# Performance work log

Hardware: AMD Instinct MI355X
Metric: run time of the kernel (lower is better)

## Reference

```python
import jax, jax.numpy as jnp
import numpy as np

K = 10
EPS = 1e-5

def leaky(x):
    return jnp.where(x >= 0, x, 0.2 * x)

def graph_feature(x, k):
    # x: (B, C, N) -> edge features (B, 2C, N, k), standard DGCNN get_graph_feature
    B, C, N = x.shape
    xx = jnp.sum(x * x, axis=1)                      # (B, N)
    inner = jnp.einsum('bcn,bcm->bnm', x, x)          # (B, N, N)
    pair = 2.0 * inner - xx[:, :, None] - xx[:, None, :]  # -||xi - xj||^2
    _, idx = jax.lax.top_k(pair, k)                   # (B, N, k)
    xt = jnp.transpose(x, (0, 2, 1))                  # (B, N, C)
    nbr = xt[jnp.arange(B)[:, None, None], idx]       # (B, N, k, C) gather
    ctr = jnp.broadcast_to(xt[:, :, None, :], nbr.shape)
    feat = jnp.concatenate([nbr - ctr, ctr], axis=-1)  # (B, N, k, 2C)
    return jnp.transpose(feat, (0, 3, 1, 2))          # (B, 2C, N, k)

def edge_block(x, W, k):
    # gather -> 1x1 conv (edge MLP) -> leaky relu -> max over neighbors
    e = graph_feature(x, k)                           # (B, 2C, N, k)
    h = leaky(jnp.einsum('oc,bcnk->bonk', W, e))      # (B, O, N, k)
    return jnp.max(h, axis=-1)                        # (B, O, N)

def bn(x, g, b, m, v):
    # inference batchnorm over channel axis 1; x: (B, C, ...) 
    shape = (1, -1) + (1,) * (x.ndim - 2)
    return (x - m.reshape(shape)) * (g.reshape(shape) * jax.lax.rsqrt(v.reshape(shape) + EPS)) + b.reshape(shape)

def setup_inputs() -> dict:
    key = jax.random.key(0)
    ks = jax.random.split(key, 20)
    s = lambda i, shape, scale: (jax.random.normal(ks[i], shape, jnp.float32) * scale)
    inp = {
        'input': jax.random.normal(ks[0], (759, 220, 3), jnp.float32),
        'W1': s(1, (32, 6), 0.4),
        'W2': s(2, (32, 64), 0.15),
        'W3': s(3, (64, 64), 0.15),
        'W4': s(4, (128, 128), 0.1),
        'W5': s(5, (512, 256), 0.08),
        'g5': 1.0 + s(6, (512,), 0.05), 'b5': s(7, (512,), 0.05),
        'm5': s(8, (512,), 0.05), 'v5': 1.0 + 0.1 * jax.random.uniform(ks[9], (512,), jnp.float32),
        'Wl1': s(10, (1024, 1024), 0.03),
        'g6': 1.0 + s(11, (1024,), 0.05), 'b6': s(12, (1024,), 0.05),
        'm6': s(13, (1024,), 0.05), 'v6': 1.0 + 0.1 * jax.random.uniform(ks[14], (1024,), jnp.float32),
        'Wl2': s(15, (380, 1024), 0.03),
        'bl2': s(16, (380,), 0.02),
    }
    return inp

def reference(input, W1, W2, W3, W4, W5, g5, b5, m5, v5, Wl1, g6, b6, m6, v6, Wl2, bl2):
    x = jnp.transpose(input.reshape(-1, 220, 3), (0, 2, 1))  # (B, 3, N)
    x1 = edge_block(x, W1, K)    # (B, 32, N)
    x2 = edge_block(x1, W2, K)   # (B, 32, N)
    x3 = edge_block(x2, W3, K)   # (B, 64, N)
    x4 = edge_block(x3, W4, K)   # (B, 128, N)
    xc = jnp.concatenate([x1, x2, x3, x4], axis=1)           # (B, 256, N)
    h = leaky(bn(jnp.einsum('oc,bcn->bon', W5, xc), g5, b5, m5, v5))  # (B, 512, N)
    p = jnp.concatenate([jnp.max(h, axis=-1), jnp.mean(h, axis=-1)], axis=1)  # (B, 1024)
    z = leaky(bn(p @ Wl1.T, g6, b6, m6, v6))  # dropout is identity in eval
    return z @ Wl2.T + bl2                     # (B, 380)
```

## Files before the change

### kernel.cpp

```cpp
#include <hip/hip_runtime.h>
#include <math.h>

#define NB 759
#define NPT 220
#define KNN 10
#define XCCH 256
#define LDXC (XCCH * NPT)

typedef float f4 __attribute__((ext_vector_type(4)));
typedef float f16v __attribute__((ext_vector_type(16)));
typedef short bf8v __attribute__((ext_vector_type(8)));

__device__ inline unsigned short bfh(float x) {
  unsigned u = __float_as_uint(x);
  unsigned r = u + 0x7FFFu + ((u >> 16) & 1u);
  return (unsigned short)(r >> 16);
}
__device__ inline float bff(unsigned short h) {
  return __uint_as_float(((unsigned)h) << 16);
}
__device__ inline void bfsplit(float x, unsigned short& h, unsigned short& l) {
  h = bfh(x);
  l = bfh(x - bff(h));
}

__global__ __launch_bounds__(256) void k_transpose(const float* __restrict__ in, float* __restrict__ x0) {
  int i = blockIdx.x * 256 + threadIdx.x;
  if (i >= NB * 3 * NPT) return;
  int n = i % NPT; int t = i / NPT; int c = t % 3; int b = t / 3;
  x0[i] = in[(b * NPT + n) * 3 + c];
}

__global__ __launch_bounds__(256) void k_w5split(const float* __restrict__ W5,
    unsigned short* __restrict__ Wh, unsigned short* __restrict__ Wl) {
  int i = blockIdx.x * 256 + threadIdx.x;
  if (i >= 512 * 256) return;
  bfsplit(W5[i], Wh[i], Wl[i]);
}

__device__ inline void topk_insert(float d, int m, float* tv, int* ti) {
  if (d > tv[KNN - 1]) {
    tv[KNN - 1] = d; ti[KNN - 1] = m;
    #pragma unroll
    for (int j = KNN - 1; j >= 1; --j) {
      if (tv[j] > tv[j - 1]) {
        float tf = tv[j - 1]; tv[j - 1] = tv[j]; tv[j] = tf;
        int tq = ti[j - 1]; ti[j - 1] = ti[j]; ti[j] = tq;
      } else break;
    }
  }
}

__global__ __launch_bounds__(256) void k_knn3(const float* __restrict__ x, int ldb,
                                              int* __restrict__ idxout) {
  __shared__ __align__(16) float xl[NPT * 4];
  __shared__ float xx[NPT];
  int b = blockIdx.x;
  const float* xb = x + (size_t)b * ldb;
  for (int i = threadIdx.x; i < NPT; i += 256) {
    f4 v; v.x = xb[i]; v.y = xb[NPT + i]; v.z = xb[2 * NPT + i]; v.w = 0.f;
    *(f4*)&xl[i * 4] = v;
    xx[i] = v.x * v.x + v.y * v.y + v.z * v.z;
  }
  __syncthreads();
  int n = threadIdx.x;
  if (n >= NPT) return;
  f4 xn = *(const f4*)&xl[n * 4];
  float xxn = xx[n];
  float tv[KNN]; int ti[KNN];
  #pragma unroll
  for (int k = 0; k < KNN; ++k) { tv[k] = -1e30f; ti[k] = 0; }
  for (int m = 0; m < NPT; ++m) {
    f4 v = *(const f4*)&xl[m * 4];
    float dot = xn.x * v.x + xn.y * v.y + xn.z * v.z;
    topk_insert(2.f * dot - xxn - xx[m], m, tv, ti);
  }
  int* ib = idxout + ((size_t)b * NPT + n) * KNN;
  #pragma unroll
  for (int k = 0; k < KNN; ++k) ib[k] = ti[k];
}

template<int C>
__global__ __launch_bounds__(512) void k_knn_mfma(const float* __restrict__ x, int ldb,
                                                  int* __restrict__ idxout) {
  constexpr int KPG = C + 8;
  constexpr int SW = (C / 16) - 1;
  __shared__ __align__(16) unsigned short XH[224 * KPG];
  __shared__ __align__(16) unsigned short XM[224 * KPG];
  __shared__ __align__(16) unsigned short XL[224 * KPG];
  __shared__ float xx[224];
  int b = blockIdx.x;
  const float* xb = x + (size_t)b * ldb;
  for (int i = threadIdx.x; i < C * 224; i += 512) {
    int c = i / 224, m = i - c * 224;
    float v = (m < NPT) ? xb[c * NPT + m] : 0.f;
    unsigned short h = bfh(v);
    float r1 = v - bff(h);
    unsigned short mm = bfh(r1);
    unsigned short l = bfh(r1 - bff(mm));
    int cs = c ^ ((m & SW) << 4);
    XH[m * KPG + cs] = h; XM[m * KPG + cs] = mm; XL[m * KPG + cs] = l;
  }
  for (int m = threadIdx.x; m < 224; m += 512) {
    float s = 0.f;
    if (m < NPT) {
      for (int c = 0; c < C; ++c) { float v = xb[c * NPT + m]; s += v * v; }
    } else s = 1e30f;
    xx[m] = s;
  }
  __syncthreads();
  int w = threadIdx.x >> 6;
  int lane = threadIdx.x & 63;
  int lc = lane & 31, hi = lane >> 5;
  float tv[KNN]; int ti[KNN];
  #pragma unroll
  for (int k = 0; k < KNN; ++k) { tv[k] = -1e30f; ti[k] = 0; }
  if (w < 7) {
    int n = w * 32 + lc;
    f16v acc[7];
    #pragma unroll
    for (int mt = 0; mt < 7; ++mt)
      #pragma unroll
      for (int i = 0; i < 16; ++i) acc[mt][i] = 0.f;
    #pragma unroll
    for (int ks = 0; ks < C / 16; ++ks) {
      int kb = ks * 16 + hi * 8;
      int nsw = kb ^ ((n & SW) << 4);
      bf8v bh = *(const bf8v*)&XH[n * KPG + nsw];
      bf8v bm = *(const bf8v*)&XM[n * KPG + nsw];
      bf8v bl = *(const bf8v*)&XL[n * KPG + nsw];
      #pragma unroll
      for (int mt = 0; mt < 7; ++mt) {
        int mr = mt * 32 + lc;
        int msw = kb ^ ((mr & SW) << 4);
        bf8v ah = *(const bf8v*)&XH[mr * KPG + msw];
        bf8v am = *(const bf8v*)&XM[mr * KPG + msw];
        bf8v al = *(const bf8v*)&XL[mr * KPG + msw];
        acc[mt] = __builtin_amdgcn_mfma_f32_32x32x16_bf16(ah, bh, acc[mt], 0, 0, 0);
        acc[mt] = __builtin_amdgcn_mfma_f32_32x32x16_bf16(am, bh, acc[mt], 0, 0, 0);
        acc[mt] = __builtin_amdgcn_mfma_f32_32x32x16_bf16(ah, bm, acc[mt], 0, 0, 0);
        acc[mt] = __builtin_amdgcn_mfma_f32_32x32x16_bf16(am, bm, acc[mt], 0, 0, 0);
        acc[mt] = __builtin_amdgcn_mfma_f32_32x32x16_bf16(al, bh, acc[mt], 0, 0, 0);
        acc[mt] = __builtin_amdgcn_mfma_f32_32x32x16_bf16(ah, bl, acc[mt], 0, 0, 0);
      }
    }
    float xxn = xx[n];
    #pragma unroll
    for (int mt = 0; mt < 7; ++mt)
      #pragma unroll
      for (int i = 0; i < 16; ++i) {
        int m = mt * 32 + (i & 3) + 8 * (i >> 2) + 4 * hi;
        float d = 2.f * acc[mt][i] - xx[m] - xxn;
        topk_insert(d, m, tv, ti);
      }
  }
  __syncthreads();
  float* LV = (float*)XH;
  int* LI = (int*)XM;
  if (w < 7) {
    int slot = (w * 64 + lane) * KNN;
    #pragma unroll
    for (int k = 0; k < KNN; ++k) { LV[slot + k] = tv[k]; LI[slot + k] = ti[k]; }
  }
  __syncthreads();
  if (w < 7 && hi == 0) {
    int n = w * 32 + lc;
    if (n < NPT) {
      int sa = (w * 64 + lane) * KNN, sb = sa + 32 * KNN;
      int a = 0, bq = 0;
      int* ob = idxout + ((size_t)b * NPT + n) * KNN;
      #pragma unroll
      for (int k = 0; k < KNN; ++k) {
        float va = LV[sa + a], vb = LV[sb + bq];
        int ia = LI[sa + a], ic = LI[sb + bq];
        bool ta = (va > vb) || (va == vb && ia < ic);
        ob[k] = ta ? ia : ic;
        if (ta) ++a; else ++bq;
      }
    }
  }
}

template<int CIN>
__global__ __launch_bounds__(256, 2) void k_conv_fused(const float* __restrict__ x, int ldb,
    const float* __restrict__ W, const int* __restrict__ idxb, float* __restrict__ xout) {
  constexpr int NPAD = 224;
  constexpr int DBS = 224;
  constexpr int REGION = 64 * DBS;
  __shared__ __align__(16) float smem[REGION + CIN * 64];
  __shared__ unsigned short idxl[NPT * KNN];
  float* xl = smem;
  float* db = smem;
  float* wl = smem + REGION;
  int b = blockIdx.x, og = blockIdx.y;
  const float* xb = x + (size_t)b * ldb;
  for (int i = threadIdx.x; i < CIN * NPAD; i += 256) {
    int c = i / NPAD, n = i - c * NPAD;
    xl[i] = (n < NPT) ? xb[c * NPT + n] : 0.f;
  }
  for (int i = threadIdx.x; i < 64 * CIN; i += 256) {
    int rl = i & 63, c = i >> 6;
    int o = og * 32 + (rl & 31);
    float wv = (rl < 32) ? W[o * 2 * CIN + c]
                         : (W[o * 2 * CIN + CIN + c] - W[o * 2 * CIN + c]);
    wl[c * 64 + rl] = wv;
  }
  for (int i = threadIdx.x; i < NPT * KNN; i += 256)
    idxl[i] = (unsigned short)idxb[(size_t)b * NPT * KNN + i];
  __syncthreads();
  int rq = threadIdx.x & 15, nq = threadIdx.x >> 4;
  int gv[4]; bool gok[4];
  #pragma unroll
  for (int j = 0; j < 4; ++j) { int g = nq + j * 16; gok[j] = g < 55; gv[j] = (g < 55 ? g : 54) * 4; }
  f4 acc[4][4];
  #pragma unroll
  for (int j = 0; j < 4; ++j)
    #pragma unroll
    for (int i2 = 0; i2 < 4; ++i2) acc[j][i2] = (f4){0.f, 0.f, 0.f, 0.f};
  #pragma unroll 2
  for (int c = 0; c < CIN; ++c) {
    f4 wv = *(const f4*)&wl[c * 64 + rq * 4];
    #pragma unroll
    for (int j = 0; j < 4; ++j) {
      f4 xv = *(const f4*)&xl[c * NPAD + gv[j]];
      acc[j][0] += wv.x * xv; acc[j][1] += wv.y * xv;
      acc[j][2] += wv.z * xv; acc[j][3] += wv.w * xv;
    }
  }
  __syncthreads();
  #pragma unroll
  for (int j = 0; j < 4; ++j) {
    if (gok[j]) {
      #pragma unroll
      for (int i2 = 0; i2 < 4; ++i2)
        *(f4*)&db[(rq * 4 + i2) * DBS + gv[j]] = acc[j][i2];
    }
  }
  __syncthreads();
  int o0 = og * 32;
  for (int i = threadIdx.x; i < 32 * NPT; i += 256) {
    int ol = i / NPT, n = i - ol * NPT;
    const float* drow = &db[ol * DBS];
    const unsigned short* ib = &idxl[n * KNN];
    float mx = -1e30f;
    #pragma unroll
    for (int k = 0; k < KNN; ++k) mx = fmaxf(mx, drow[ib[k]]);
    float v = mx + db[(32 + ol) * DBS + n];
    xout[((size_t)b * XCCH + o0 + ol) * NPT + n] = (v >= 0.f) ? v : 0.2f * v;
  }
}

#define KP 72
__global__ __launch_bounds__(256) void k_w5_mfma(const float* __restrict__ xc,
    const unsigned short* __restrict__ Wh, const unsigned short* __restrict__ Wl,
    const float* __restrict__ g5, const float* __restrict__ b5, const float* __restrict__ m5,
    const float* __restrict__ v5, float* __restrict__ p) {
  __shared__ __align__(16) unsigned short XH[224 * KP];
  __shared__ __align__(16) unsigned short XL[224 * KP];
  int d = blockIdx.x;
  int b = (d & 7) * 95 + (d >> 5);
  int rg = (d >> 3) & 3;
  if (b >= NB) return;
  int lane = threadIdx.x & 63, w = threadIdx.x >> 6;
  f16v acc[7];
  #pragma unroll
  for (int t = 0; t < 7; ++t)
    #pragma unroll
    for (int i = 0; i < 16; ++i) acc[t][i] = 0.f;

  int r = rg * 128 + w * 32 + (lane & 31);
  int khalf = (lane >> 5) * 8;

  for (int cb = 0; cb < 4; ++cb) {
    if (cb) __syncthreads();
    for (int i = threadIdx.x; i < 32 * NPT; i += 256) {
      int cp = i / NPT;
      int n = i - cp * NPT;
      int c0 = cp * 2;
      const float* src = &xc[((size_t)b * XCCH + cb * 64 + c0) * NPT + n];
      float x0 = src[0];
      float x1 = src[NPT];
      unsigned short h0, l0, h1, l1;
      bfsplit(x0, h0, l0); bfsplit(x1, h1, l1);
      ((unsigned*)XH)[(n * KP + c0) >> 1] = (unsigned)h0 | ((unsigned)h1 << 16);
      ((unsigned*)XL)[(n * KP + c0) >> 1] = (unsigned)l0 | ((unsigned)l1 << 16);
    }
    for (int i = threadIdx.x; i < 4 * 32; i += 256) {
      int n = NPT + (i >> 5); int cd = i & 31;
      ((unsigned*)XH)[n * (KP / 2) + cd] = 0u;
      ((unsigned*)XL)[n * (KP / 2) + cd] = 0u;
    }
    __syncthreads();
    #pragma unroll
    for (int ks = 0; ks < 4; ++ks) {
      int kg = cb * 64 + ks * 16 + khalf;
      int kl = ks * 16 + khalf;
      bf8v ah = *(const bf8v*)&Wh[(size_t)r * 256 + kg];
      bf8v al = *(const bf8v*)&Wl[(size_t)r * 256 + kg];
      #pragma unroll
      for (int t = 0; t < 7; ++t) {
        int col = t * 32 + (lane & 31);
        bf8v bh = *(const bf8v*)&XH[col * KP + kl];
        bf8v bl = *(const bf8v*)&XL[col * KP + kl];
        acc[t] = __builtin_amdgcn_mfma_f32_32x32x16_bf16(ah, bh, acc[t], 0, 0, 0);
        acc[t] = __builtin_amdgcn_mfma_f32_32x32x16_bf16(al, bh, acc[t], 0, 0, 0);
        acc[t] = __builtin_amdgcn_mfma_f32_32x32x16_bf16(ah, bl, acc[t], 0, 0, 0);
      }
    }
  }
  int rbase = rg * 128 + w * 32 + 4 * (lane >> 5);
  int lc = lane & 31;
  #pragma unroll
  for (int i = 0; i < 16; ++i) {
    int row = rbase + (i & 3) + 8 * (i >> 2);
    float a = g5[row] * rsqrtf(v5[row] + 1e-5f);
    float dq = b5[row] - m5[row] * a;
    float mx = -1e30f, sm = 0.f;
    #pragma unroll
    for (int t = 0; t < 7; ++t) {
      bool valid = (t < 6) || (lc < 28);
      float hv = a * acc[t][i] + dq;
      float lv = (hv >= 0.f) ? hv : 0.2f * hv;
      if (valid) { mx = fmaxf(mx, lv); sm += lv; }
    }
    #pragma unroll
    for (int m_ = 1; m_ <= 16; m_ <<= 1) {
      mx = fmaxf(mx, __shfl_xor(mx, m_));
      sm += __shfl_xor(sm, m_);
    }
    if (lc == 0) {
      p[(size_t)b * 1024 + row] = mx;
      p[(size_t)b * 1024 + 512 + row] = sm * (1.f / NPT);
    }
  }
}

template<int ON, bool FUSE>
__global__ __launch_bounds__(256) void k_fc(const float* __restrict__ in, const float* __restrict__ Wt,
    const float* __restrict__ q0, const float* __restrict__ q1, const float* __restrict__ q2,
    const float* __restrict__ q3, float* __restrict__ out, int ostride) {
  __shared__ __align__(16) float il[32 * 68];
  __shared__ __align__(16) float wl[32 * 68];
  int b0 = blockIdx.x * 64, o0 = blockIdx.y * 64;
  int oq = threadIdx.x & 15, bq = threadIdx.x >> 4;
  f4 acc[4];
  #pragma unroll
  for (int i2 = 0; i2 < 4; ++i2) acc[i2] = (f4){0.f, 0.f, 0.f, 0.f};
  for (int cb = 0; cb < 32; ++cb) {
    if (cb) __syncthreads();
    for (int i = threadIdx.x; i < 2048; i += 256) {
      int c = i & 31, bb = i >> 5;
      il[c * 68 + bb] = (b0 + bb < NB) ? in[(b0 + bb) * 1024 + cb * 32 + c] : 0.f;
    }
    for (int i = threadIdx.x; i < 2048; i += 256) {
      int c = i & 31, ol = i >> 5;
      wl[c * 68 + ol] = (o0 + ol < ON) ? Wt[(o0 + ol) * 1024 + cb * 32 + c] : 0.f;
    }
    __syncthreads();
    #pragma unroll
    for (int c = 0; c < 32; ++c) {
      f4 wv = *(const f4*)&wl[c * 68 + oq * 4];
      f4 iv = *(const f4*)&il[c * 68 + bq * 4];
      acc[0] += wv.x * iv; acc[1] += wv.y * iv; acc[2] += wv.z * iv; acc[3] += wv.w * iv;
    }
  }
  #pragma unroll
  for (int i2 = 0; i2 < 4; ++i2) {
    int o = o0 + oq * 4 + i2;
    if (o >= ON) continue;
    float A = 1.f, Dv = 0.f;
    if (FUSE) { float a = q0[o] * rsqrtf(q3[o] + 1e-5f); A = a; Dv = q1[o] - q2[o] * a; }
    else { Dv = q0[o]; }
    #pragma unroll
    for (int jj = 0; jj < 4; ++jj) {
      int bb = b0 + bq * 4 + jj;
      if (bb < NB) {
        float v = acc[i2][jj];
        if (FUSE) { v = A * v + Dv; v = (v >= 0.f) ? v : 0.2f * v; }
        else { v = v + Dv; }
        out[(size_t)bb * ostride + o] = v;
      }
    }
  }
}

extern "C" void kernel_launch(void* const* d_in, const int* in_sizes, int n_in,
                              void* d_out, int out_size, void* d_ws, size_t ws_size,
                              hipStream_t stream) {
  const float* input = (const float*)d_in[0];
  const float* W1 = (const float*)d_in[1];
  const float* W2 = (const float*)d_in[2];
  const float* W3 = (const float*)d_in[3];
  const float* W4 = (const float*)d_in[4];
  const float* W5 = (const float*)d_in[5];
  const float* g5 = (const float*)d_in[6];
  const float* b5 = (const float*)d_in[7];
  const float* m5 = (const float*)d_in[8];
  const float* v5 = (const float*)d_in[9];
  const float* Wl1 = (const float*)d_in[10];
  const float* g6 = (const float*)d_in[11];
  const float* b6 = (const float*)d_in[12];
  const float* m6 = (const float*)d_in[13];
  const float* v6 = (const float*)d_in[14];
  const float* Wl2 = (const float*)d_in[15];
  const float* bl2 = (const float*)d_in[16];

  float* w = (float*)d_ws;
  float* x0 = w;
  float* xc = x0 + 500940;
  float* p  = xc + 42746880;
  float* z  = p  + 777216;
  int* idxb = (int*)(z + 777216);
  unsigned short* wh = (unsigned short*)(w + 46472052);
  unsigned short* wlo = wh + 131072;

  k_transpose<<<1957, 256, 0, stream>>>(input, x0);
  k_w5split<<<512, 256, 0, stream>>>(W5, wh, wlo);

  k_knn3<<<759, 256, 0, stream>>>(x0, 3 * NPT, idxb);
  k_conv_fused<3><<<dim3(759, 1), 256, 0, stream>>>(x0, 3 * NPT, W1, idxb, xc);

  k_knn_mfma<32><<<759, 512, 0, stream>>>(xc, LDXC, idxb);
  k_conv_fused<32><<<dim3(759, 1), 256, 0, stream>>>(xc, LDXC, W2, idxb, xc + 32 * NPT);

  k_knn_mfma<32><<<759, 512, 0, stream>>>(xc + 32 * NPT, LDXC, idxb);
  k_conv_fused<32><<<dim3(759, 2), 256, 0, stream>>>(xc + 32 * NPT, LDXC, W3, idxb, xc + 64 * NPT);

  k_knn_mfma<64><<<759, 512, 0, stream>>>(xc + 64 * NPT, LDXC, idxb);
  k_conv_fused<64><<<dim3(759, 4), 256, 0, stream>>>(xc + 64 * NPT, LDXC, W4, idxb, xc + 128 * NPT);

  k_w5_mfma<<<3040, 256, 0, stream>>>(xc, wh, wlo, g5, b5, m5, v5, p);

  k_fc<1024, true><<<dim3(12, 16), 256, 0, stream>>>(p, Wl1, g6, b6, m6, v6, z, 1024);
  k_fc<380, false><<<dim3(12, 6), 256, 0, stream>>>(z, Wl2, bl2, bl2, bl2, bl2, (float*)d_out, 380);
}
```

Baseline: 1.698 ms.

## Restructure W5 MFMA kernel: 512 threads, waves split over columns, swizzled LDS

The W5 pointwise-conv kernel now runs 512 threads per block. Each of 7 active waves owns one 32-column slice of points and loops over 4 row tiles, where before each of 4 waves owned a row slice and swept all 7 column tiles. The padded LDS layout (KP=72) becomes an XOR-swizzled 64-wide layout to avoid bank conflicts. BN scale and shift are precomputed once into shared memory, and the max/mean reduction is finished through a shared buffer across waves. This cuts accumulator registers per wave and reuses each LDS B fragment across 4 row tiles. In exchange, one of the 8 waves sits idle during compute, W fragments are reloaded from global memory more often, and an extra sync plus shared-memory reduction is added.

```diff
diff --git a/kernel.cpp b/kernel.cpp
--- a/kernel.cpp
+++ b/kernel.cpp
@@ -250,30 +250,37 @@
   }
 }
 
-#define KP 72
-__global__ __launch_bounds__(256) void k_w5_mfma(const float* __restrict__ xc,
+__global__ __launch_bounds__(512, 4) void k_w5_mfma(const float* __restrict__ xc,
     const unsigned short* __restrict__ Wh, const unsigned short* __restrict__ Wl,
     const float* __restrict__ g5, const float* __restrict__ b5, const float* __restrict__ m5,
     const float* __restrict__ v5, float* __restrict__ p) {
-  __shared__ __align__(16) unsigned short XH[224 * KP];
-  __shared__ __align__(16) unsigned short XL[224 * KP];
+  __shared__ __align__(16) unsigned short XH[224 * 64];
+  __shared__ __align__(16) unsigned short XL[224 * 64];
+  __shared__ float red[128][8][2];
+  __shared__ float ADq[128][2];
   int d = blockIdx.x;
   int b = (d & 7) * 95 + (d >> 5);
   int rg = (d >> 3) & 3;
   if (b >= NB) return;
   int lane = threadIdx.x & 63, w = threadIdx.x >> 6;
-  f16v acc[7];
-  #pragma unroll
-  for (int t = 0; t < 7; ++t)
-    #pragma unroll
-    for (int i = 0; i < 16; ++i) acc[t][i] = 0.f;
-
-  int r = rg * 128 + w * 32 + (lane & 31);
-  int khalf = (lane >> 5) * 8;
+  int lc = lane & 31, hi = lane >> 5;
+
+  if (threadIdx.x < 128) {
+    int row = rg * 128 + threadIdx.x;
+    float a = g5[row] * rsqrtf(v5[row] + 1e-5f);
+    ADq[threadIdx.x][0] = a;
+    ADq[threadIdx.x][1] = b5[row] - m5[row] * a;
+  }
+
+  f16v acc[4];
+  #pragma unroll
+  for (int rt = 0; rt < 4; ++rt)
+    #pragma unroll
+    for (int i = 0; i < 16; ++i) acc[rt][i] = 0.f;
 
   for (int cb = 0; cb < 4; ++cb) {
     if (cb) __syncthreads();
-    for (int i = threadIdx.x; i < 32 * NPT; i += 256) {
+    for (int i = threadIdx.x; i < 32 * NPT; i += 512) {
       int cp = i / NPT;
       int n = i - cp * NPT;
       int c0 = cp * 2;
@@ -282,56 +289,71 @@
       float x1 = src[NPT];
       unsigned short h0, l0, h1, l1;
       bfsplit(x0, h0, l0); bfsplit(x1, h1, l1);
-      ((unsigned*)XH)[(n * KP + c0) >> 1] = (unsigned)h0 | ((unsigned)h1 << 16);
-      ((unsigned*)XL)[(n * KP + c0) >> 1] = (unsigned)l0 | ((unsigned)l1 << 16);
-    }
-    for (int i = threadIdx.x; i < 4 * 32; i += 256) {
+      int dw = n * 32 + (((c0 >> 3) ^ (n & 7)) << 2) + ((c0 & 7) >> 1);
+      ((unsigned*)XH)[dw] = (unsigned)h0 | ((unsigned)h1 << 16);
+      ((unsigned*)XL)[dw] = (unsigned)l0 | ((unsigned)l1 << 16);
+    }
+    for (int i = threadIdx.x; i < 128; i += 512) {
       int n = NPT + (i >> 5); int cd = i & 31;
-      ((unsigned*)XH)[n * (KP / 2) + cd] = 0u;
-      ((unsigned*)XL)[n * (KP / 2) + cd] = 0u;
+      ((unsigned*)XH)[n * 32 + cd] = 0u;
+      ((unsigned*)XL)[n * 32 + cd] = 0u;
     }
     __syncthreads();
-    #pragma unroll
-    for (int ks = 0; ks < 4; ++ks) {
-      int kg = cb * 64 + ks * 16 + khalf;
-      int kl = ks * 16 + khalf;
-      bf8v ah = *(const bf8v*)&Wh[(size_t)r * 256 + kg];
-      bf8v al = *(const bf8v*)&Wl[(size_t)r * 256 + kg];
-      #pragma unroll
-      for (int t = 0; t < 7; ++t) {
-        int col = t * 32 + (lane & 31);
-        bf8v bh = *(const bf8v*)&XH[col * KP + kl];
-        bf8v bl = *(const bf8v*)&XL[col * KP + kl];
-        acc[t] = __builtin_amdgcn_mfma_f32_32x32x16_bf16(ah, bh, acc[t], 0, 0, 0);
-        acc[t] = __builtin_amdgcn_mfma_f32_32x32x16_bf16(al, bh, acc[t], 0, 0, 0);
-        acc[t] = __builtin_amdgcn_mfma_f32_32x32x16_bf16(ah, bl, acc[t], 0, 0, 0);
-      }
-    }
-  }
-  int rbase = rg * 128 + w * 32 + 4 * (lane >> 5);
-  int lc = lane & 31;
-  #pragma unroll
-  for (int i = 0; i < 16; ++i) {
-    int row = rbase + (i & 3) + 8 * (i >> 2);
-    float a = g5[row] * rsqrtf(v5[row] + 1e-5f);
-    float dq = b5[row] - m5[row] * a;
+    if (w < 7) {
+      int col = w * 32 + lc;
+      int swc = col & 7;
+      const unsigned short* XHr = &XH[col * 64];
+      const unsigned short* XLr = &XL[col * 64];
+      #pragma unroll
+      for (int ks = 0; ks < 4; ++ks) {
+        int gr = (((ks * 2 + hi) ^ swc) << 3);
+        bf8v bh = *(const bf8v*)&XHr[gr];
+        bf8v bl = *(const bf8v*)&XLr[gr];
+        int kg = cb * 64 + ks * 16 + hi * 8;
+        const unsigned short* wp = Wh + (size_t)(rg * 128 + lc) * 256 + kg;
+        const unsigned short* wq = Wl + (size_t)(rg * 128 + lc) * 256 + kg;
+        #pragma unroll
+        for (int rt = 0; rt < 4; ++rt) {
+          bf8v ah = *(const bf8v*)(wp + rt * 32 * 256);
+          bf8v al = *(const bf8v*)(wq + rt * 32 * 256);
+          acc[rt] = __builtin_amdgcn_mfma_f32_32x32x16_bf16(ah, bh, acc[rt], 0, 0, 0);
+          acc[rt] = __builtin_amdgcn_mfma_f32_32x32x16_bf16(al, bh, acc[rt], 0, 0, 0);
+          acc[rt] = __builtin_amdgcn_mfma_f32_32x32x16_bf16(ah, bl, acc[rt], 0, 0, 0);
+        }
+      }
+    }
+  }
+  if (w < 7) {
+    bool allv = (w < 6);
+    #pragma unroll
+    for (int rt = 0; rt < 4; ++rt) {
+      #pragma unroll
+      for (int i = 0; i < 16; ++i) {
+        int rl = rt * 32 + (i & 3) + 8 * (i >> 2) + 4 * hi;
+        float a = ADq[rl][0], dq = ADq[rl][1];
+        float hv = a * acc[rt][i] + dq;
+        float lv = (hv >= 0.f) ? hv : 0.2f * hv;
+        bool valid = allv || (lc < 28);
+        float mx = valid ? lv : -1e30f;
+        float sm = valid ? lv : 0.f;
+        #pragma unroll
+        for (int m_ = 1; m_ <= 16; m_ <<= 1) {
+          mx = fmaxf(mx, __shfl_xor(mx, m_));
+          sm += __shfl_xor(sm, m_);
+        }
+        if (lc == 0) { red[rl][w][0] = mx; red[rl][w][1] = sm; }
+      }
+    }
+  }
+  __syncthreads();
+  if (threadIdx.x < 128) {
+    int rl = threadIdx.x;
     float mx = -1e30f, sm = 0.f;
     #pragma unroll
-    for (int t = 0; t < 7; ++t) {
-      bool valid = (t < 6) || (lc < 28);
-      float hv = a * acc[t][i] + dq;
-      float lv = (hv >= 0.f) ? hv : 0.2f * hv;
-      if (valid) { mx = fmaxf(mx, lv); sm += lv; }
-    }
-    #pragma unroll
-    for (int m_ = 1; m_ <= 16; m_ <<= 1) {
-      mx = fmaxf(mx, __shfl_xor(mx, m_));
-      sm += __shfl_xor(sm, m_);
-    }
-    if (lc == 0) {
-      p[(size_t)b * 1024 + row] = mx;
-      p[(size_t)b * 1024 + 512 + row] = sm * (1.f / NPT);
-    }
+    for (int q = 0; q < 7; ++q) { mx = fmaxf(mx, red[rl][q][0]); sm += red[rl][q][1]; }
+    int row = rg * 128 + rl;
+    p[(size_t)b * 1024 + row] = mx;
+    p[(size_t)b * 1024 + 512 + row] = sm * (1.f / NPT);
   }
 }
 
@@ -429,7 +451,7 @@
   k_knn_mfma<64><<<759, 512, 0, stream>>>(xc + 64 * NPT, LDXC, idxb);
   k_conv_fused<64><<<dim3(759, 4), 256, 0, stream>>>(xc + 64 * NPT, LDXC, W4, idxb, xc + 128 * NPT);
 
-  k_w5_mfma<<<3040, 256, 0, stream>>>(xc, wh, wlo, g5, b5, m5, v5, p);
+  k_w5_mfma<<<3040, 512, 0, stream>>>(xc, wh, wlo, g5, b5, m5, v5, p);
 
   k_fc<1024, true><<<dim3(12, 16), 256, 0, stream>>>(p, Wl1, g6, b6, m6, v6, z, 1024);
   k_fc<380, false><<<dim3(12, 6), 256, 0, stream>>>(z, Wl2, bl2, bl2, bl2, bl2, (float*)d_out, 380);
```

Result: slower. 1.901 ms (+11.9%).

## Emit pre-split bf16 hi/lo xc in MFMA layout from edge-conv kernels

Applied to the files above, without the earlier changes.

Each edge-conv epilogue now also writes its output as pre-split bf16 high/low halves in a channel-group-of-8 interleaved layout that the W5 MFMA kernel can copy straight into shared memory with vector loads. A new W5 kernel streams 32-channel chunks from this layout instead of loading fp32 xc and splitting it itself, and the last conv skips its fp32 write. The aim is to remove the fp32-to-bf16 conversion and transpose work from the W5 kernel. The cost is extra global writes in every conv, a large extra workspace, and a fallback path used when the workspace is too small.

```diff
diff --git a/kernel.cpp b/kernel.cpp
--- a/kernel.cpp
+++ b/kernel.cpp
@@ -10,6 +10,7 @@
 typedef float f4 __attribute__((ext_vector_type(4)));
 typedef float f16v __attribute__((ext_vector_type(16)));
 typedef short bf8v __attribute__((ext_vector_type(8)));
+typedef unsigned u4v __attribute__((ext_vector_type(4)));
 
 __device__ inline unsigned short bfh(float x) {
   unsigned u = __float_as_uint(x);
@@ -181,9 +182,10 @@
   }
 }
 
-template<int CIN>
+template<int CIN, bool WBF16, bool WF32>
 __global__ __launch_bounds__(256, 2) void k_conv_fused(const float* __restrict__ x, int ldb,
-    const float* __restrict__ W, const int* __restrict__ idxb, float* __restrict__ xout) {
+    const float* __restrict__ W, const int* __restrict__ idxb, float* __restrict__ xout,
+    unsigned short* __restrict__ xch, unsigned short* __restrict__ xcl, int cbase) {
   constexpr int NPAD = 224;
   constexpr int DBS = 224;
   constexpr int REGION = 64 * DBS;
@@ -238,15 +240,104 @@
   }
   __syncthreads();
   int o0 = og * 32;
-  for (int i = threadIdx.x; i < 32 * NPT; i += 256) {
-    int ol = i / NPT, n = i - ol * NPT;
-    const float* drow = &db[ol * DBS];
-    const unsigned short* ib = &idxl[n * KNN];
-    float mx = -1e30f;
-    #pragma unroll
-    for (int k = 0; k < KNN; ++k) mx = fmaxf(mx, drow[ib[k]]);
-    float v = mx + db[(32 + ol) * DBS + n];
-    xout[((size_t)b * XCCH + o0 + ol) * NPT + n] = (v >= 0.f) ? v : 0.2f * v;
+  for (int i = threadIdx.x; i < 32 * 224; i += 256) {
+    int ol = i / 224, n = i - ol * 224;
+    unsigned short h = 0, l = 0;
+    if (n < NPT) {
+      const float* drow = &db[ol * DBS];
+      const unsigned short* ib = &idxl[n * KNN];
+      float mx = -1e30f;
+      #pragma unroll
+      for (int k = 0; k < KNN; ++k) mx = fmaxf(mx, drow[ib[k]]);
+      float v = mx + db[(32 + ol) * DBS + n];
+      v = (v >= 0.f) ? v : 0.2f * v;
+      if (WF32) xout[((size_t)b * XCCH + o0 + ol) * NPT + n] = v;
+      if (WBF16) bfsplit(v, h, l);
+    }
+    if (WBF16) {
+      int c = cbase + o0 + ol;
+      size_t off = (((size_t)b * 32 + (c >> 3)) * 224 + n) * 8 + (c & 7);
+      xch[off] = h;
+      xcl[off] = l;
+    }
+  }
+}
+
+__global__ __launch_bounds__(256) void k_w5_mfma_ps(
+    const unsigned short* __restrict__ xch, const unsigned short* __restrict__ xcl,
+    const unsigned short* __restrict__ Wh, const unsigned short* __restrict__ Wl,
+    const float* __restrict__ g5, const float* __restrict__ b5, const float* __restrict__ m5,
+    const float* __restrict__ v5, float* __restrict__ p) {
+  __shared__ __align__(16) unsigned short XH[4 * 224 * 8];
+  __shared__ __align__(16) unsigned short XL[4 * 224 * 8];
+  int d = blockIdx.x;
+  int b = (d & 7) * 95 + (d >> 5);
+  int rg = (d >> 3) & 3;
+  if (b >= NB) return;
+  int lane = threadIdx.x & 63, w = threadIdx.x >> 6;
+  f16v acc[7];
+  #pragma unroll
+  for (int t = 0; t < 7; ++t)
+    #pragma unroll
+    for (int i = 0; i < 16; ++i) acc[t][i] = 0.f;
+
+  int r = rg * 128 + w * 32 + (lane & 31);
+  int khalf = (lane >> 5) * 8;
+  const u4v* srcH = (const u4v*)(xch + (size_t)b * 57344);
+  const u4v* srcL = (const u4v*)(xcl + (size_t)b * 57344);
+  u4v* dH = (u4v*)XH;
+  u4v* dL = (u4v*)XL;
+
+  for (int cb = 0; cb < 8; ++cb) {
+    if (cb) __syncthreads();
+    const u4v* sH = srcH + cb * 896;
+    const u4v* sL = srcL + cb * 896;
+    for (int i = threadIdx.x; i < 896; i += 256) {
+      dH[i] = sH[i];
+      dL[i] = sL[i];
+    }
+    __syncthreads();
+    #pragma unroll
+    for (int ks = 0; ks < 2; ++ks) {
+      int kg = cb * 32 + ks * 16 + khalf;
+      int g = ks * 2 + (lane >> 5);
+      bf8v ah = *(const bf8v*)&Wh[(size_t)r * 256 + kg];
+      bf8v al = *(const bf8v*)&Wl[(size_t)r * 256 + kg];
+      #pragma unroll
+      for (int t = 0; t < 7; ++t) {
+        int col = t * 32 + (lane & 31);
+        bf8v bh = *(const bf8v*)&XH[g * 1792 + col * 8];
+        bf8v bl = *(const bf8v*)&XL[g * 1792 + col * 8];
+        acc[t] = __builtin_amdgcn_mfma_f32_32x32x16_bf16(ah, bh, acc[t], 0, 0, 0);
+        acc[t] = __builtin_amdgcn_mfma_f32_32x32x16_bf16(al, bh, acc[t], 0, 0, 0);
+        acc[t] = __builtin_amdgcn_mfma_f32_32x32x16_bf16(ah, bl, acc[t], 0, 0, 0);
+      }
+    }
+  }
+  int rbase = rg * 128 + w * 32 + 4 * (lane >> 5);
+  int lc = lane & 31;
+  #pragma unroll
+  for (int i = 0; i < 16; ++i) {
+    int row = rbase + (i & 3) + 8 * (i >> 2);
+    float a = g5[row] * rsqrtf(v5[row] + 1e-5f);
+    float dq = b5[row] - m5[row] * a;
+    float mx = -1e30f, sm = 0.f;
+    #pragma unroll
+    for (int t = 0; t < 7; ++t) {
+      bool valid = (t < 6) || (lc < 28);
+      float hv = a * acc[t][i] + dq;
+      float lv = (hv >= 0.f) ? hv : 0.2f * hv;
+      if (valid) { mx = fmaxf(mx, lv); sm += lv; }
+    }
+    #pragma unroll
+    for (int m_ = 1; m_ <= 16; m_ <<= 1) {
+      mx = fmaxf(mx, __shfl_xor(mx, m_));
+      sm += __shfl_xor(sm, m_);
+    }
+    if (lc == 0) {
+      p[(size_t)b * 1024 + row] = mx;
+      p[(size_t)b * 1024 + 512 + row] = sm * (1.f / NPT);
+    }
   }
 }
 
@@ -413,23 +504,35 @@
   int* idxb = (int*)(z + 777216);
   unsigned short* wh = (unsigned short*)(w + 46472052);
   unsigned short* wlo = wh + 131072;
+  unsigned short* xch = wlo + 131072;
+  unsigned short* xcl = xch + 43524096;
+  size_t need = (size_t)(xcl + 43524096 - (unsigned short*)d_ws) * 2;
+  bool ps = ws_size >= need;
 
   k_transpose<<<1957, 256, 0, stream>>>(input, x0);
   k_w5split<<<512, 256, 0, stream>>>(W5, wh, wlo);
 
   k_knn3<<<759, 256, 0, stream>>>(x0, 3 * NPT, idxb);
-  k_conv_fused<3><<<dim3(759, 1), 256, 0, stream>>>(x0, 3 * NPT, W1, idxb, xc);
-
-  k_knn_mfma<32><<<759, 512, 0, stream>>>(xc, LDXC, idxb);
-  k_conv_fused<32><<<dim3(759, 1), 256, 0, stream>>>(xc, LDXC, W2, idxb, xc + 32 * NPT);
-
-  k_knn_mfma<32><<<759, 512, 0, stream>>>(xc + 32 * NPT, LDXC, idxb);
-  k_conv_fused<32><<<dim3(759, 2), 256, 0, stream>>>(xc + 32 * NPT, LDXC, W3, idxb, xc + 64 * NPT);
-
-  k_knn_mfma<64><<<759, 512, 0, stream>>>(xc + 64 * NPT, LDXC, idxb);
-  k_conv_fused<64><<<dim3(759, 4), 256, 0, stream>>>(xc + 64 * NPT, LDXC, W4, idxb, xc + 128 * NPT);
-
-  k_w5_mfma<<<3040, 256, 0, stream>>>(xc, wh, wlo, g5, b5, m5, v5, p);
+
+  if (ps) {
+    k_conv_fused<3, true, true><<<dim3(759, 1), 256, 0, stream>>>(x0, 3 * NPT, W1, idxb, xc, xch, xcl, 0);
+    k_knn_mfma<32><<<759, 512, 0, stream>>>(xc, LDXC, idxb);
+    k_conv_fused<32, true, true><<<dim3(759, 1), 256, 0, stream>>>(xc, LDXC, W2, idxb, xc + 32 * NPT, xch, xcl, 32);
+    k_knn_mfma<32><<<759, 512, 0, stream>>>(xc + 32 * NPT, LDXC, idxb);
+    k_conv_fused<32, true, true><<<dim3(759, 2), 256, 0, stream>>>(xc + 32 * NPT, LDXC, W3, idxb, xc + 64 * NPT, xch, xcl, 64);
+    k_knn_mfma<64><<<759, 512, 0, stream>>>(xc + 64 * NPT, LDXC, idxb);
+    k_conv_fused<64, true, false><<<dim3(759, 4), 256, 0, stream>>>(xc + 64 * NPT, LDXC, W4, idxb, xc + 128 * NPT, xch, xcl, 128);
+    k_w5_mfma_ps<<<3040, 256, 0, stream>>>(xch, xcl, wh, wlo, g5, b5, m5, v5, p);
+  } else {
+    k_conv_fused<3, false, true><<<dim3(759, 1), 256, 0, stream>>>(x0, 3 * NPT, W1, idxb, xc, xch, xcl, 0);
+    k_knn_mfma<32><<<759, 512, 0, stream>>>(xc, LDXC, idxb);
+    k_conv_fused<32, false, true><<<dim3(759, 1), 256, 0, stream>>>(xc, LDXC, W2, idxb, xc + 32 * NPT, xch, xcl, 32);
+    k_knn_mfma<32><<<759, 512, 0, stream>>>(xc + 32 * NPT, LDXC, idxb);
+    k_conv_fused<32, false, true><<<dim3(759, 2), 256, 0, stream>>>(xc + 32 * NPT, LDXC, W3, idxb, xc + 64 * NPT, xch, xcl, 64);
+    k_knn_mfma<64><<<759, 512, 0, stream>>>(xc + 64 * NPT, LDXC, idxb);
+    k_conv_fused<64, false, true><<<dim3(759, 4), 256, 0, stream>>>(xc + 64 * NPT, LDXC, W4, idxb, xc + 128 * NPT, xch, xcl, 128);
+    k_w5_mfma<<<3040, 256, 0, stream>>>(xc, wh, wlo, g5, b5, m5, v5, p);
+  }
 
   k_fc<1024, true><<<dim3(12, 16), 256, 0, stream>>>(p, Wl1, g6, b6, m6, v6, z, 1024);
   k_fc<380, false><<<dim3(12, 6), 256, 0, stream>>>(z, Wl2, bl2, bl2, bl2, bl2, (float*)d_out, 380);
```

After: 1.721 ms. About the same (+1.3%).
